# Kernel optimization log

Hardware: AMD Instinct MI355X
Metric: run time of the kernel (lower is better)

## Reference

```python
import jax, jax.numpy as jnp
import numpy as np
from jax import lax

B, S, D, H = 512, 120, 216, 1024
MAX_LEN = 24


def setup_inputs() -> dict:
    key = jax.random.key(0)
    ks = jax.random.split(key, 8)
    u = lambda k, shape: jax.random.uniform(k, shape, jnp.float32, -0.08, 0.08)  # init_weights
    return {
        "src": jax.random.normal(ks[0], (B, S, D), jnp.float32),
        "W_ih": u(ks[1], (4 * H, D)),
        "W_hh": u(ks[2], (4 * H, H)),
        "b_ih": u(ks[3], (4 * H,)),
        "b_hh": u(ks[4], (4 * H,)),
        "W_out": u(ks[5], (D, H)),
        "b_out": u(ks[6], (D,)),
        "max_len": MAX_LEN,
    }


def _lstm_cell(x, h, c, W_ih, W_hh, b):
    # PyTorch gate order: i, f, g, o
    gates = x @ W_ih.T + h @ W_hh.T + b  # (B, 4H)
    i, f, g, o = jnp.split(gates, 4, axis=-1)
    c_new = jax.nn.sigmoid(f) * c + jax.nn.sigmoid(i) * jnp.tanh(g)
    h_new = jax.nn.sigmoid(o) * jnp.tanh(c_new)
    return h_new, c_new


def reference(src, W_ih, W_hh, b_ih, b_hh, W_out, b_out, max_len):
    # Eval-mode forward: dropout off; encoder teacher-forced over src;
    b = b_ih + b_hh
    src_t = jnp.swapaxes(src, 0, 1)  # (S, B, D)
    Bsz = src.shape[0]
    Hd = W_hh.shape[1]
    h0 = jnp.zeros((Bsz, Hd), src.dtype)
    c0 = jnp.zeros((Bsz, Hd), src.dtype)

    def enc_step(carry, x_t):
        h, c = carry
        h, c = _lstm_cell(x_t, h, c, W_ih, W_hh, b)
        return (h, c), None

    (h, c), _ = lax.scan(enc_step, (h0, c0), src_t)

    def dec_step(carry, _):
        h, c, inp = carry
        h, c = _lstm_cell(inp, h, c, W_ih, W_hh, b)
        y = h @ W_out.T + b_out  # project_to_output
        return (h, c, y), y

    (_, _, _), ys = lax.scan(dec_step, (h, c, src_t[-1]), None, length=max_len)
    return jnp.swapaxes(ys, 0, 1)  # (B, max_len, D)
```

## Files before the change

### kernel.cpp

```cpp
#include <hip/hip_runtime.h>
#include <cstdint>
#include <cstddef>

#define B_SZ 512
#define S_SZ 120
#define D_SZ 216
#define H_SZ 1024
#define NG   4096
#define DP   256
#define KENC 1280
#define TMAX 24

#define BM 64
#define BN 128
#define BK 64
#define NBUF 5

using bf16_t = __bf16;
using bf16x8 = __attribute__((ext_vector_type(8))) __bf16;
using f32x4  = __attribute__((ext_vector_type(4))) float;

__device__ __forceinline__ void gload16(const void* g, void* l) {
  __builtin_amdgcn_global_load_lds(
      (const __attribute__((address_space(1))) void*)g,
      (__attribute__((address_space(3))) void*)l, 16, 0, 0);
}
__device__ __forceinline__ void gload16c(const void* g, void* l) {
  __builtin_amdgcn_global_load_lds(
      (const __attribute__((address_space(1))) void*)g,
      (__attribute__((address_space(3))) void*)l, 16, 0, 0x11);
}

__device__ __forceinline__ float fsigmoid(float x) {
  x = fminf(fmaxf(x, -30.f), 30.f);
  return 1.f / (1.f + __expf(-x));
}
__device__ __forceinline__ float ftanh(float x) {
  x = fminf(fmaxf(x, -15.f), 15.f);
  float e = __expf(2.f * x);
  return (e - 1.f) / (e + 1.f);
}

#define BUFB 24576
struct __align__(16) Smem {
  bf16_t stage[NBUF][(BM + BN) * BK];
  float gate[BM * 129];
};

__global__ __launch_bounds__(512, 1) void lstm_chain(
    const bf16_t* __restrict__ srcbf,
    const bf16_t* __restrict__ Wcat,
    const bf16_t* __restrict__ Wdec,
    const float* __restrict__ biasE,
    const float* __restrict__ biasD,
    float* __restrict__ cbuf,
    bf16_t* __restrict__ hA,
    bf16_t* __restrict__ hB,
    bf16_t* __restrict__ Hs,
    unsigned* __restrict__ flags)
{
  __shared__ Smem sm;
  const int t    = threadIdx.x;
  const int bid  = blockIdx.x;
  const int n0   = (bid & 31) * BN;
  const int m0   = (bid >> 5) * BM;
  const int lane = t & 63;
  const int wv   = t >> 6;
  const int wm   = wv >> 2;
  const int wn   = wv & 3;
  const int fr   = lane & 15;
  const int fq   = lane >> 4;

  char* ldsbase = (char*)&sm.stage[0][0];

  const int sgrp = lane >> 3;
  const int sw8  = (((lane & 7) ^ sgrp) & 7) * 8;
  const int aRowOff = 8 * wv + sgrp;
  const int wRowOff = 16 * wv + sgrp;

  const int swz   = fr & 7;
  const int co0   = ((fq) ^ swz) * 16;
  const int co1   = ((4 + fq) ^ swz) * 16;
  const int arow0 = (wm * 32 + fr) * 128;
  const int arow1 = (wm * 32 + 16 + fr) * 128;
  const int brow  = 8192 + (wn * 32 + fr) * 128;
  const int u0    = n0 >> 2;

  const int panel = m0 >> 6;
  unsigned* flg = flags + panel * 32;
  unsigned* myf = flg + (n0 >> 7);
  const unsigned* myFlagAddr = flg + (lane & 31);

  auto stageSlice = [&](const bf16_t* Ab, int sA, int ka, bool coh,
                        const bf16_t* Wb, int sW2, int kw, int buf) {
    char* lb = ldsbase + buf * BUFB;
    const bf16_t* ap = Ab + (size_t)(m0 + aRowOff) * sA + sw8 + ka;
    if (coh) gload16c(ap, lb + wv * 1024);
    else     gload16 (ap, lb + wv * 1024);
    const bf16_t* wp = Wb + (size_t)(n0 + wRowOff) * sW2 + sw8 + kw;
    gload16(wp, lb + 8192 + wv * 2048);
    gload16(wp + (size_t)8 * sW2, lb + 8192 + wv * 2048 + 1024);
  };

  f32x4 acc[2][2];

  auto compute = [&](int bf) {
    const char* Lb = ldsbase + bf * BUFB;
#pragma unroll
    for (int kk = 0; kk < 2; ++kk) {
      const int co = kk ? co1 : co0;
      bf16x8 av0 = *(const bf16x8*)(Lb + arow0 + co);
      bf16x8 av1 = *(const bf16x8*)(Lb + arow1 + co);
      bf16x8 bv0 = *(const bf16x8*)(Lb + brow + co);
      bf16x8 bv1 = *(const bf16x8*)(Lb + brow + 2048 + co);
      acc[0][0] = __builtin_amdgcn_mfma_f32_16x16x32_bf16(av0, bv0, acc[0][0], 0, 0, 0);
      acc[0][1] = __builtin_amdgcn_mfma_f32_16x16x32_bf16(av0, bv1, acc[0][1], 0, 0, 0);
      acc[1][0] = __builtin_amdgcn_mfma_f32_16x16x32_bf16(av1, bv0, acc[1][0], 0, 0, 0);
      acc[1][1] = __builtin_amdgcn_mfma_f32_16x16x32_bf16(av1, bv1, acc[1][1], 0, 0, 0);
    }
  };

  auto panelSpin = [&](unsigned need) {
    asm volatile("s_waitcnt vmcnt(0)" ::: "memory");
    for (;;) {
      unsigned v;
      asm volatile("global_load_dword %0, %1, off sc0 sc1\n\t"
                   "s_waitcnt vmcnt(0)"
                   : "=v"(v) : "v"(myFlagAddr) : "memory");
      if (__all((int)(v >= need))) break;
      __builtin_amdgcn_s_sleep(2);
    }
  };

  const bf16_t* hprev = hA;
  int cb = 0;

  stageSlice(srcbf, DP, 0,      false, Wcat, KENC, 0,      0);
  stageSlice(srcbf, DP, BK,     false, Wcat, KENC, BK,     1);
  stageSlice(srcbf, DP, 2 * BK, false, Wcat, KENC, 2 * BK, 2);
  stageSlice(srcbf, DP, 3 * BK, false, Wcat, KENC, 3 * BK, 3);

#pragma clang loop unroll(disable)
  for (int s = 0; s < 144; ++s) {
    const bool enc = (s <= 120);
    const int  xi  = (s < 120) ? s : 119;
    const bf16_t* Asrc = srcbf + (size_t)xi * B_SZ * DP;
    const int n1 = enc ? (DP / BK) : 0;
    const bf16_t* Wb  = enc ? Wcat : Wdec;
    const int     sWb = enc ? KENC : H_SZ;
    const float*  bias = enc ? biasE : biasD;
    bf16_t* hnext = (s < 120) ? ((s & 1) ? hA : hB)
                              : (Hs + (size_t)(s - 120) * B_SZ * H_SZ);
    const int nTot = n1 + H_SZ / BK;
    const bool nxtEnc = (s + 1 <= 120);
    const bool crossA = (s < 143) && nxtEnc;
    const bf16_t* nxtW  = nxtEnc ? Wcat : Wdec;
    const int     nxtsW = nxtEnc ? KENC : H_SZ;
    const bf16_t* nxtA  = srcbf + (size_t)((s + 1 < 120) ? (s + 1) : 119) * B_SZ * DP;

    float bias2[2];
#pragma unroll
    for (int j = 0; j < 2; ++j) bias2[j] = bias[n0 + wn * 32 + j * 16 + fr];

#pragma unroll
    for (int i = 0; i < 2; ++i)
#pragma unroll
      for (int j = 0; j < 2; ++j) acc[i][j] = (f32x4){0.f, 0.f, 0.f, 0.f};

    for (int it = 0; it < nTot; ++it) {
      const int rem = nTot - it;
      if (crossA || rem >= 4)
        asm volatile("s_waitcnt vmcnt(9)" ::: "memory");
      else if (rem == 3)
        asm volatile("s_waitcnt vmcnt(6)" ::: "memory");
      else if (rem == 2)
        asm volatile("s_waitcnt vmcnt(3)" ::: "memory");
      else
        asm volatile("s_waitcnt vmcnt(0)" ::: "memory");
      __builtin_amdgcn_s_barrier();

      const int j4 = it + 4;
      const int sbuf = (cb + 4 >= NBUF) ? cb - 1 : cb + 4;

      if (j4 < nTot) {
        if (j4 < n1) {
          stageSlice(Asrc, DP, j4 * BK, false, Wb, sWb, j4 * BK, sbuf);
        } else {
          if (enc && j4 == n1 && s > 0) panelSpin((unsigned)s);
          stageSlice(hprev, H_SZ, (j4 - n1) * BK, true, Wb, sWb, j4 * BK, sbuf);
        }
      } else if (crossA) {
        const int q = j4 - nTot;
        stageSlice(nxtA, DP, q * BK, false, nxtW, nxtsW, q * BK, sbuf);
      }

      compute(cb);
      cb = (cb == NBUF - 1) ? 0 : cb + 1;
    }

#pragma unroll
    for (int i = 0; i < 2; ++i)
#pragma unroll
      for (int j = 0; j < 2; ++j)
#pragma unroll
        for (int v = 0; v < 4; ++v) {
          int row = wm * 32 + i * 16 + fq * 4 + v;
          int col = wn * 32 + j * 16 + fr;
          sm.gate[row * 129 + col] = acc[i][j][v] + bias2[j];
        }
    __syncthreads();
#pragma unroll
    for (int itc = 0; itc < 4; ++itc) {
      int ci  = itc * 512 + t;
      int brw = ci >> 5;
      int ju  = ci & 31;
      const float* gp = &sm.gate[brw * 129 + ju * 4];
      float iv = fsigmoid(gp[0]);
      float fv = fsigmoid(gp[1]);
      float gv = ftanh(gp[2]);
      float ov = fsigmoid(gp[3]);
      size_t cix = (size_t)(m0 + brw) * H_SZ + (u0 + ju);
      float cn = fv * cbuf[cix] + iv * gv;
      cbuf[cix] = cn;
      bf16_t hb = (bf16_t)(ov * ftanh(cn));
      uint32_t hv32 = (uint32_t)__builtin_bit_cast(uint16_t, hb);
      asm volatile("global_store_short %0, %1, off sc0 sc1"
                   :: "v"((uint16_t*)&hnext[cix]), "v"(hv32) : "memory");
    }
    asm volatile("s_waitcnt vmcnt(0)" ::: "memory");
    __syncthreads();
    if (t == 0) {
      unsigned fv2 = (unsigned)(s + 1);
      asm volatile("global_store_dword %0, %1, off sc0 sc1"
                   :: "v"(myf), "v"(fv2) : "memory");
    }

    if (s < 143 && !nxtEnc) {
      panelSpin((unsigned)(s + 1));
      int b = cb;
#pragma unroll
      for (int q = 0; q < 4; ++q) {
        stageSlice(hnext, H_SZ, q * BK, true, Wdec, H_SZ, q * BK, b);
        b = (b == NBUF - 1) ? 0 : b + 1;
      }
    }

    hprev = hnext;
  }
}

template <int EPI>
__global__ __launch_bounds__(256, 1) void gemm_step(
    const bf16_t* __restrict__ A1, int sA1, int n1,
    const bf16_t* __restrict__ A2, int sA2, int n2,
    const bf16_t* __restrict__ W, int sW,
    const float* __restrict__ bias,
    float* __restrict__ cbuf, bf16_t* __restrict__ hout,
    const float* __restrict__ addm, bf16_t* __restrict__ outb,
    float* __restrict__ outf)
{
  __shared__ Smem sm;
  const int t    = threadIdx.x;
  const int m0   = blockIdx.y * BM;
  const int n0   = blockIdx.x * BN;
  const int lane = t & 63;
  const int wv   = t >> 6;
  const int wm   = wv >> 1, wn = wv & 1;
  const int fr   = lane & 15;
  const int fq   = lane >> 4;

  f32x4 acc[2][4] = {};

  float bias4[4];
  if (EPI == 1 || EPI == 3) {
#pragma unroll
    for (int j = 0; j < 4; ++j) {
      int col = n0 + wn * 64 + j * 16 + fr;
      bias4[j] = (EPI == 3 && col >= D_SZ) ? 0.f : bias[col];
    }
  }

  const int r0   = t >> 3;
  const int gcol = (((t & 7) ^ (r0 & 7)) * 8);
  char* ldsbase  = (char*)&sm.stage[0][0];
  const int wofs = wv * 1024;

  const bf16_t* pA1 = A1 ? A1 : A2;
  const bf16_t* pA2 = A2 ? A2 : A1;
  const bf16_t* a1p0 = pA1 + (size_t)(m0 + r0) * sA1 + gcol;
  const bf16_t* a1p1 = pA1 + (size_t)(m0 + r0 + 32) * sA1 + gcol;
  const bf16_t* a2p0 = pA2 + (size_t)(m0 + r0) * sA2 + gcol;
  const bf16_t* a2p1 = pA2 + (size_t)(m0 + r0 + 32) * sA2 + gcol;
  const bf16_t* wp0  = W + (size_t)(n0 + r0) * sW + gcol;
  const bf16_t* wp1  = W + (size_t)(n0 + r0 + 32) * sW + gcol;
  const bf16_t* wp2  = W + (size_t)(n0 + r0 + 64) * sW + gcol;
  const bf16_t* wp3  = W + (size_t)(n0 + r0 + 96) * sW + gcol;

  const int nTot = n1 + n2;

  auto stage = [&](int j, int bf) {
    char* Ab = ldsbase + bf * BUFB + wofs;
    char* Bb = ldsbase + bf * BUFB + 8192 + wofs;
    const int k = j * BK;
    const bf16_t *a0, *a1;
    if (j < n1) { a0 = a1p0 + k; a1 = a1p1 + k; }
    else { const int k2 = k - n1 * BK; a0 = a2p0 + k2; a1 = a2p1 + k2; }
    gload16(a0, Ab);
    gload16(a1, Ab + 4096);
    gload16(wp0 + k, Bb);
    gload16(wp1 + k, Bb + 4096);
    gload16(wp2 + k, Bb + 8192);
    gload16(wp3 + k, Bb + 12288);
  };

  const int swz  = fr & 7;
  const int co0  = ((fq) ^ swz) * 16;
  const int co1  = ((4 + fq) ^ swz) * 16;
  const int arow0 = (wm * 32 + fr) * 128;
  const int arow1 = (wm * 32 + 16 + fr) * 128;
  const int brow  = (wn * 64 + fr) * 128;

  auto compute = [&](int bf) {
    const char* Ab = ldsbase + bf * BUFB;
    const char* Bb = Ab + 8192;
#pragma unroll
    for (int kk = 0; kk < 2; ++kk) {
      const int co = kk ? co1 : co0;
      bf16x8 av0 = *(const bf16x8*)(Ab + arow0 + co);
      bf16x8 av1 = *(const bf16x8*)(Ab + arow1 + co);
      bf16x8 bv[4];
#pragma unroll
      for (int j = 0; j < 4; ++j)
        bv[j] = *(const bf16x8*)(Bb + brow + j * 2048 + co);
#pragma unroll
      for (int j = 0; j < 4; ++j) {
        acc[0][j] = __builtin_amdgcn_mfma_f32_16x16x32_bf16(av0, bv[j], acc[0][j], 0, 0, 0);
        acc[1][j] = __builtin_amdgcn_mfma_f32_16x16x32_bf16(av1, bv[j], acc[1][j], 0, 0, 0);
      }
    }
  };

  stage(0, 0);
  if (nTot > 1) stage(1, 1);
  int cb = 0, sb = 2;
  for (int it = 0; it < nTot; ++it) {
    if (it == nTot - 1) {
      asm volatile("s_waitcnt vmcnt(0)" ::: "memory");
    } else {
      asm volatile("s_waitcnt vmcnt(6)" ::: "memory");
    }
    __builtin_amdgcn_s_barrier();
    if (it + 2 < nTot) stage(it + 2, sb);
    sb = (sb == 2) ? 0 : sb + 1;
    compute(cb);
    cb = (cb == 2) ? 0 : cb + 1;
  }
  __syncthreads();

  if (EPI == 1) {
#pragma unroll
    for (int i = 0; i < 2; ++i)
#pragma unroll
      for (int j = 0; j < 4; ++j)
#pragma unroll
        for (int v = 0; v < 4; ++v) {
          int row = wm * 32 + i * 16 + fq * 4 + v;
          int col = wn * 64 + j * 16 + fr;
          sm.gate[row * 129 + col] = acc[i][j][v] + bias4[j];
        }
    __syncthreads();
    const int u0 = n0 >> 2;
#pragma unroll
    for (int itc = 0; itc < 8; ++itc) {
      int ci = itc * 256 + t;
      int brw = ci >> 5;
      int ju  = ci & 31;
      const float* gp = &sm.gate[brw * 129 + ju * 4];
      float iv = fsigmoid(gp[0]);
      float fv = fsigmoid(gp[1]);
      float gv = ftanh(gp[2]);
      float ov = fsigmoid(gp[3]);
      size_t cix = (size_t)(m0 + brw) * H_SZ + (u0 + ju);
      float cn = fv * cbuf[cix] + iv * gv;
      cbuf[cix] = cn;
      hout[cix] = (bf16_t)(ov * ftanh(cn));
    }
  }

  if (EPI == 2) {
#pragma unroll
    for (int i = 0; i < 2; ++i)
#pragma unroll
      for (int j = 0; j < 4; ++j)
#pragma unroll
        for (int v = 0; v < 4; ++v) {
          int gr = m0 + wm * 32 + i * 16 + fq * 4 + v;
          int gc = n0 + wn * 64 + j * 16 + fr;
          int orig = (gr & 3) * H_SZ + (gr >> 2);
          float val = acc[i][j][v] + addm[(size_t)orig * H_SZ + gc];
          outb[(size_t)gr * H_SZ + gc] = (bf16_t)val;
        }
  }

  if (EPI == 3) {
#pragma unroll
    for (int i = 0; i < 2; ++i)
#pragma unroll
      for (int j = 0; j < 4; ++j)
#pragma unroll
        for (int v = 0; v < 4; ++v) {
          int m = m0 + wm * 32 + i * 16 + fq * 4 + v;
          int n = n0 + wn * 64 + j * 16 + fr;
          if (n < D_SZ) {
            int ts = m >> 9;
            int bb = m & 511;
            outf[((size_t)bb * TMAX + ts) * D_SZ + n] = acc[i][j][v] + bias4[j];
          }
        }
  }
}

__global__ void k_convert_src(const float* __restrict__ src, bf16_t* __restrict__ dst) {
  int idx = blockIdx.x * 256 + threadIdx.x;
  int total = S_SZ * B_SZ * DP;
  if (idx >= total) return;
  int d = idx % DP;
  int r = idx / DP;
  int b = r % B_SZ;
  int tt = r / B_SZ;
  float v = (d < D_SZ) ? src[((size_t)b * S_SZ + tt) * D_SZ + d] : 0.f;
  dst[idx] = (bf16_t)v;
}

__global__ void k_build_wcat(const float* __restrict__ Wih, const float* __restrict__ Whh,
                             bf16_t* __restrict__ Wcat) {
  int idx = blockIdx.x * 256 + threadIdx.x;
  if (idx >= NG * KENC) return;
  int k = idx % KENC;
  int r = idx / KENC;
  int o = (r & 3) * H_SZ + (r >> 2);
  float v;
  if (k < D_SZ)      v = Wih[(size_t)o * D_SZ + k];
  else if (k < DP)   v = 0.f;
  else               v = Whh[(size_t)o * H_SZ + (k - DP)];
  Wcat[idx] = (bf16_t)v;
}

__global__ void k_build_wout(const float* __restrict__ Wout, bf16_t* __restrict__ WoutB,
                             bf16_t* __restrict__ WoutT) {
  int idx = blockIdx.x * 256 + threadIdx.x;
  if (idx < 256 * H_SZ) {
    int h = idx % H_SZ, d = idx / H_SZ;
    WoutB[idx] = (bf16_t)((d < D_SZ) ? Wout[(size_t)d * H_SZ + h] : 0.f);
  }
  if (idx < H_SZ * DP) {
    int d = idx % DP, h = idx / DP;
    WoutT[idx] = (bf16_t)((d < D_SZ) ? Wout[(size_t)d * H_SZ + h] : 0.f);
  }
}

__global__ void k_build_bias(const float* __restrict__ bih, const float* __restrict__ bhh,
                             const float* __restrict__ Wih, const float* __restrict__ bout,
                             float* __restrict__ biasE, float* __restrict__ biasD) {
  int r = blockIdx.x * 256 + threadIdx.x;
  if (r >= NG) return;
  int o = (r & 3) * H_SZ + (r >> 2);
  float be = bih[o] + bhh[o];
  biasE[r] = be;
  float s = 0.f;
  const float* wr = Wih + (size_t)o * D_SZ;
  for (int d = 0; d < D_SZ; ++d) s += wr[d] * bout[d];
  biasD[r] = be + s;
}

extern "C" void kernel_launch(void* const* d_in, const int* in_sizes, int n_in,
                              void* d_out, int out_size, void* d_ws, size_t ws_size,
                              hipStream_t stream) {
  const float* src  = (const float*)d_in[0];
  const float* Wih  = (const float*)d_in[1];
  const float* Whh  = (const float*)d_in[2];
  const float* bih  = (const float*)d_in[3];
  const float* bhh  = (const float*)d_in[4];
  const float* Wout = (const float*)d_in[5];
  const float* bout = (const float*)d_in[6];

  char* ws = (char*)d_ws;
  size_t off = 0;
  auto alloc = [&](size_t bytes) {
    void* p = ws + off;
    off = (off + bytes + 255) & ~(size_t)255;
    return p;
  };
  bf16_t* srcbf = (bf16_t*)alloc((size_t)S_SZ * B_SZ * DP * 2);
  bf16_t* Wcat  = (bf16_t*)alloc((size_t)NG * KENC * 2);
  bf16_t* Wdec  = (bf16_t*)alloc((size_t)NG * H_SZ * 2);
  bf16_t* WoutB = (bf16_t*)alloc((size_t)256 * H_SZ * 2);
  bf16_t* WoutT = (bf16_t*)alloc((size_t)H_SZ * DP * 2);
  float*  biasE = (float*)alloc((size_t)NG * 4);
  float*  biasD = (float*)alloc((size_t)NG * 4);
  float*  cbuf  = (float*)alloc((size_t)B_SZ * H_SZ * 4);
  bf16_t* hP0   = (bf16_t*)alloc((size_t)B_SZ * H_SZ * 2);
  bf16_t* hP1   = (bf16_t*)alloc((size_t)B_SZ * H_SZ * 2);
  bf16_t* Hs    = (bf16_t*)alloc((size_t)TMAX * B_SZ * H_SZ * 2);
  unsigned* flags = (unsigned*)alloc(1024);

  hipMemsetAsync(cbuf, 0, (size_t)B_SZ * H_SZ * 4, stream);
  hipMemsetAsync(hP0, 0, (size_t)B_SZ * H_SZ * 2, stream);
  hipMemsetAsync(flags, 0, 1024, stream);

  k_convert_src<<<(S_SZ * B_SZ * DP + 255) / 256, 256, 0, stream>>>(src, srcbf);
  k_build_wcat<<<(NG * KENC + 255) / 256, 256, 0, stream>>>(Wih, Whh, Wcat);
  k_build_wout<<<1024, 256, 0, stream>>>(Wout, WoutB, WoutT);
  k_build_bias<<<(NG + 255) / 256, 256, 0, stream>>>(bih, bhh, Wih, bout, biasE, biasD);

  gemm_step<2><<<dim3(H_SZ / BN, NG / BM), 256, 0, stream>>>(
      Wcat, KENC, DP / BK, nullptr, 0, 0, WoutT, DP,
      nullptr, nullptr, nullptr, Whh, Wdec, nullptr);

  {
    const bf16_t* a_src = srcbf;
    const bf16_t* a_wc  = Wcat;
    const bf16_t* a_wd  = Wdec;
    const float*  a_bE  = biasE;
    const float*  a_bD  = biasD;
    float*        a_cb  = cbuf;
    bf16_t*       a_hA  = hP0;
    bf16_t*       a_hB  = hP1;
    bf16_t*       a_Hs  = Hs;
    unsigned*     a_fl  = flags;
    void* kargs[] = {&a_src, &a_wc, &a_wd, &a_bE, &a_bD,
                     &a_cb, &a_hA, &a_hB, &a_Hs, &a_fl};
    hipLaunchCooperativeKernel((void*)lstm_chain, dim3(256), dim3(512),
                               kargs, 0, stream);
  }

  gemm_step<3><<<dim3(2, (TMAX * B_SZ) / BM), 256, 0, stream>>>(
      nullptr, 0, 0, Hs, H_SZ, H_SZ / BK, WoutB, H_SZ,
      bout, nullptr, nullptr, nullptr, nullptr, (float*)d_out);
}
```

Baseline: 1.898 ms.

## Keep LSTM cell state in registers and restructure cross-step prefetch and spin

```diff
diff --git a/kernel.cpp b/kernel.cpp
--- a/kernel.cpp
+++ b/kernel.cpp
@@ -42,9 +42,17 @@
 }
 
 #define BUFB 24576
-struct __align__(16) Smem {
+
+struct __align__(16) SmemChain {
   bf16_t stage[NBUF][(BM + BN) * BK];
-  float gate[BM * 129];
+  float gate[BM * 132];
+};
+
+struct __align__(16) SmemG {
+  union {
+    bf16_t stage[3][(BM + BN) * BK];
+    float gate[BM * 129];
+  };
 };
 
 __global__ __launch_bounds__(512, 1) void lstm_chain(
@@ -53,13 +61,12 @@
     const bf16_t* __restrict__ Wdec,
     const float* __restrict__ biasE,
     const float* __restrict__ biasD,
-    float* __restrict__ cbuf,
     bf16_t* __restrict__ hA,
     bf16_t* __restrict__ hB,
     bf16_t* __restrict__ Hs,
     unsigned* __restrict__ flags)
 {
-  __shared__ Smem sm;
+  __shared__ SmemChain sm;
   const int t    = threadIdx.x;
   const int bid  = blockIdx.x;
   const int n0   = (bid & 31) * BN;
@@ -121,7 +128,6 @@
   };
 
   auto panelSpin = [&](unsigned need) {
-    asm volatile("s_waitcnt vmcnt(0)" ::: "memory");
     for (;;) {
       unsigned v;
       asm volatile("global_load_dword %0, %1, off sc0 sc1\n\t"
@@ -131,6 +137,15 @@
       __builtin_amdgcn_s_sleep(2);
     }
   };
+
+  float c4[4] = {0.f, 0.f, 0.f, 0.f};
+  float biasE2[2], biasD2[2];
+#pragma unroll
+  for (int j = 0; j < 2; ++j) {
+    int col = n0 + wn * 32 + j * 16 + fr;
+    biasE2[j] = biasE[col];
+    biasD2[j] = biasD[col];
+  }
 
   const bf16_t* hprev = hA;
   int cb = 0;
@@ -148,19 +163,13 @@
     const int n1 = enc ? (DP / BK) : 0;
     const bf16_t* Wb  = enc ? Wcat : Wdec;
     const int     sWb = enc ? KENC : H_SZ;
-    const float*  bias = enc ? biasE : biasD;
     bf16_t* hnext = (s < 120) ? ((s & 1) ? hA : hB)
                               : (Hs + (size_t)(s - 120) * B_SZ * H_SZ);
     const int nTot = n1 + H_SZ / BK;
-    const bool nxtEnc = (s + 1 <= 120);
-    const bool crossA = (s < 143) && nxtEnc;
-    const bf16_t* nxtW  = nxtEnc ? Wcat : Wdec;
-    const int     nxtsW = nxtEnc ? KENC : H_SZ;
-    const bf16_t* nxtA  = srcbf + (size_t)((s + 1 < 120) ? (s + 1) : 119) * B_SZ * DP;
 
     float bias2[2];
 #pragma unroll
-    for (int j = 0; j < 2; ++j) bias2[j] = bias[n0 + wn * 32 + j * 16 + fr];
+    for (int j = 0; j < 2; ++j) bias2[j] = enc ? biasE2[j] : biasD2[j];
 
 #pragma unroll
     for (int i = 0; i < 2; ++i)
@@ -169,7 +178,7 @@
 
     for (int it = 0; it < nTot; ++it) {
       const int rem = nTot - it;
-      if (crossA || rem >= 4)
+      if (rem >= 4)
         asm volatile("s_waitcnt vmcnt(9)" ::: "memory");
       else if (rem == 3)
         asm volatile("s_waitcnt vmcnt(6)" ::: "memory");
@@ -180,18 +189,10 @@
       __builtin_amdgcn_s_barrier();
 
       const int j4 = it + 4;
-      const int sbuf = (cb + 4 >= NBUF) ? cb - 1 : cb + 4;
-
       if (j4 < nTot) {
-        if (j4 < n1) {
-          stageSlice(Asrc, DP, j4 * BK, false, Wb, sWb, j4 * BK, sbuf);
-        } else {
-          if (enc && j4 == n1 && s > 0) panelSpin((unsigned)s);
-          stageSlice(hprev, H_SZ, (j4 - n1) * BK, true, Wb, sWb, j4 * BK, sbuf);
-        }
-      } else if (crossA) {
-        const int q = j4 - nTot;
-        stageSlice(nxtA, DP, q * BK, false, nxtW, nxtsW, q * BK, sbuf);
+        int sbuf = cb + 4; if (sbuf >= NBUF) sbuf -= NBUF;
+        if (j4 < n1) stageSlice(Asrc, DP, j4 * BK, false, Wb, sWb, j4 * BK, sbuf);
+        else         stageSlice(hprev, H_SZ, (j4 - n1) * BK, true, Wb, sWb, j4 * BK, sbuf);
       }
 
       compute(cb);
@@ -206,7 +207,7 @@
         for (int v = 0; v < 4; ++v) {
           int row = wm * 32 + i * 16 + fq * 4 + v;
           int col = wn * 32 + j * 16 + fr;
-          sm.gate[row * 129 + col] = acc[i][j][v] + bias2[j];
+          sm.gate[row * 132 + col] = acc[i][j][v] + bias2[j];
         }
     __syncthreads();
 #pragma unroll
@@ -214,16 +215,16 @@
       int ci  = itc * 512 + t;
       int brw = ci >> 5;
       int ju  = ci & 31;
-      const float* gp = &sm.gate[brw * 129 + ju * 4];
-      float iv = fsigmoid(gp[0]);
-      float fv = fsigmoid(gp[1]);
-      float gv = ftanh(gp[2]);
-      float ov = fsigmoid(gp[3]);
-      size_t cix = (size_t)(m0 + brw) * H_SZ + (u0 + ju);
-      float cn = fv * cbuf[cix] + iv * gv;
-      cbuf[cix] = cn;
+      f32x4 g = *(const f32x4*)&sm.gate[brw * 132 + ju * 4];
+      float iv = fsigmoid(g[0]);
+      float fv = fsigmoid(g[1]);
+      float gv = ftanh(g[2]);
+      float ov = fsigmoid(g[3]);
+      float cn = fv * c4[itc] + iv * gv;
+      c4[itc] = cn;
       bf16_t hb = (bf16_t)(ov * ftanh(cn));
       uint32_t hv32 = (uint32_t)__builtin_bit_cast(uint16_t, hb);
+      size_t cix = (size_t)(m0 + brw) * H_SZ + (u0 + ju);
       asm volatile("global_store_short %0, %1, off sc0 sc1"
                    :: "v"((uint16_t*)&hnext[cix]), "v"(hv32) : "memory");
     }
@@ -235,13 +236,25 @@
                    :: "v"(myf), "v"(fv2) : "memory");
     }
 
-    if (s < 143 && !nxtEnc) {
-      panelSpin((unsigned)(s + 1));
-      int b = cb;
-#pragma unroll
-      for (int q = 0; q < 4; ++q) {
-        stageSlice(hnext, H_SZ, q * BK, true, Wdec, H_SZ, q * BK, b);
-        b = (b == NBUF - 1) ? 0 : b + 1;
+    if (s < 143) {
+      const bool nxtEnc = (s + 1 <= 120);
+      if (nxtEnc) {
+        const bf16_t* nxtA = srcbf + (size_t)((s + 1 < 120) ? (s + 1) : 119) * B_SZ * DP;
+        int b = cb;
+#pragma unroll
+        for (int q = 0; q < 4; ++q) {
+          stageSlice(nxtA, DP, q * BK, false, Wcat, KENC, q * BK, b);
+          b = (b == NBUF - 1) ? 0 : b + 1;
+        }
+        panelSpin((unsigned)(s + 1));
+      } else {
+        panelSpin((unsigned)(s + 1));
+        int b = cb;
+#pragma unroll
+        for (int q = 0; q < 4; ++q) {
+          stageSlice(hnext, H_SZ, q * BK, true, Wdec, H_SZ, q * BK, b);
+          b = (b == NBUF - 1) ? 0 : b + 1;
+        }
       }
     }
 
@@ -259,7 +272,7 @@
     const float* __restrict__ addm, bf16_t* __restrict__ outb,
     float* __restrict__ outf)
 {
-  __shared__ Smem sm;
+  __shared__ SmemG sm;
   const int t    = threadIdx.x;
   const int m0   = blockIdx.y * BM;
   const int n0   = blockIdx.x * BN;
@@ -504,7 +517,6 @@
   bf16_t* Hs    = (bf16_t*)alloc((size_t)TMAX * B_SZ * H_SZ * 2);
   unsigned* flags = (unsigned*)alloc(1024);
 
-  hipMemsetAsync(cbuf, 0, (size_t)B_SZ * H_SZ * 4, stream);
   hipMemsetAsync(hP0, 0, (size_t)B_SZ * H_SZ * 2, stream);
   hipMemsetAsync(flags, 0, 1024, stream);
 
@@ -523,13 +535,12 @@
     const bf16_t* a_wd  = Wdec;
     const float*  a_bE  = biasE;
     const float*  a_bD  = biasD;
-    float*        a_cb  = cbuf;
     bf16_t*       a_hA  = hP0;
     bf16_t*       a_hB  = hP1;
     bf16_t*       a_Hs  = Hs;
     unsigned*     a_fl  = flags;
     void* kargs[] = {&a_src, &a_wc, &a_wd, &a_bE, &a_bD,
-                     &a_cb, &a_hA, &a_hB, &a_Hs, &a_fl};
+                     &a_hA, &a_hB, &a_Hs, &a_fl};
     hipLaunchCooperativeKernel((void*)lstm_chain, dim3(256), dim3(512),
                                kargs, 0, stream);
   }
```

Measured after the change: 1.731 ms. -8.8%, faster.
